# Kernel optimization log

Measured on AMD Instinct MI355X. Metric: run time of the kernel, lower is better.

Reference implementation:

```python
import jax, jax.numpy as jnp
from jax import lax
import numpy as np

B, T, F, H, L, HOR = 512, 512, 16, 256, 3, 24


def setup_inputs() -> dict:
    key = jax.random.key(0)
    ks = jax.random.split(key, 9)
    s = 0.05
    x = jax.random.normal(ks[0], (B, T, F), dtype=jnp.float32)
    # PyTorch LSTM params: gate order (i, f, g, o), W_ih [4H, in], W_hh [4H, H]
    W_ih0 = jax.random.normal(ks[1], (4 * H, F), dtype=jnp.float32) * s
    W_ih12 = jax.random.normal(ks[2], (L - 1, 4 * H, H), dtype=jnp.float32) * s
    W_hh = jax.random.normal(ks[3], (L, 4 * H, H), dtype=jnp.float32) * s
    b_ih = jax.random.normal(ks[4], (L, 4 * H), dtype=jnp.float32) * s
    b_hh = jax.random.normal(ks[5], (L, 4 * H), dtype=jnp.float32) * s
    fc_W = jax.random.normal(ks[6], (HOR, H), dtype=jnp.float32) * s
    fc_b = jax.random.normal(ks[7], (HOR,), dtype=jnp.float32) * s
    return {"x": x, "W_ih0": W_ih0, "W_ih12": W_ih12, "W_hh": W_hh,
            "b_ih": b_ih, "b_hh": b_hh, "fc_W": fc_W, "fc_b": fc_b}


def _lstm_layer(x, W_ih, W_hh, b_ih, b_hh):
    # x: [B, T, in] -> h sequence [B, T, H]
    Bn = x.shape[0]
    Hn = W_hh.shape[1]
    # precompute input contribution for all timesteps (one big GEMM)
    xg = jnp.einsum('bti,gi->btg', x, W_ih) + b_ih  # [B, T, 4H]
    W_hh_T = W_hh.T  # [H, 4H]

    def step(carry, xg_t):
        h, c = carry
        gates = xg_t + h @ W_hh_T + b_hh  # [B, 4H]
        i, f, g, o = jnp.split(gates, 4, axis=-1)
        c = jax.nn.sigmoid(f) * c + jax.nn.sigmoid(i) * jnp.tanh(g)
        h = jax.nn.sigmoid(o) * jnp.tanh(c)
        return (h, c), h

    h0 = jnp.zeros((Bn, Hn), x.dtype)
    c0 = jnp.zeros((Bn, Hn), x.dtype)
    _, hs = lax.scan(step, (h0, c0), jnp.swapaxes(xg, 0, 1))  # [T, B, H]
    return jnp.swapaxes(hs, 0, 1)


def reference(x, W_ih0, W_ih12, W_hh, b_ih, b_hh, fc_W, fc_b):
    h = _lstm_layer(x, W_ih0, W_hh[0], b_ih[0], b_hh[0])
    for l in range(1, L):
        h = _lstm_layer(h, W_ih12[l - 1], W_hh[l], b_ih[l], b_hh[l])
    last_hidden = h[:, -1, :]  # [B, H]
    return last_hidden @ fc_W.T + fc_b  # [B, horizon]
```

## Files before the change

### kernel.cpp

```cpp
#include <hip/hip_runtime.h>
#include <hip/hip_bf16.h>
#include <stdint.h>

#define Bsz 512
#define Tsz 512
#define Fsz 16
#define Hsz 256
#define HORZ 24

#define NG 8
#define NBT 8
#define BT 64
#define USL 32
#define PD 8
#define HBUF_ELEMS ((size_t)3*PD*Bsz*Hsz)
#define NFLAGS (3*NG*NBT)
#define AROW_B 512
#define ABUF_B (BT*AROW_B)
#define HTILE_B (BT*64)
#define SMEM_B (3*ABUF_B + HTILE_B)

#define POISON   0x7FC07FC0u
#define POISON64 0x7FC07FC07FC07FC0ull

typedef float  f32x4  __attribute__((ext_vector_type(4)));
typedef float  f32x16 __attribute__((ext_vector_type(16)));
typedef __bf16 bf16x8 __attribute__((ext_vector_type(8)));
typedef uint32_t u32x2 __attribute__((ext_vector_type(2)));
typedef uint32_t u32x4 __attribute__((ext_vector_type(4)));

__device__ __forceinline__ float sigm(float v){ return 1.f/(1.f+__expf(-v)); }

__device__ __forceinline__ bf16x8 ld_sc01_b128(const void* p){
  bf16x8 r;
  asm volatile("global_load_dwordx4 %0, %1, off sc0 sc1" : "=&v"(r) : "v"(p) : "memory");
  return r;
}
__device__ __forceinline__ u32x2 ld_b64_async(const void* p){
  u32x2 r;
  asm volatile("global_load_dwordx2 %0, %1, off" : "=&v"(r) : "v"(p) : "memory");
  return r;
}
__device__ __forceinline__ void st_sc01_b64(void* p, uint64_t v){
  asm volatile("global_store_dwordx2 %0, %1, off sc0 sc1" :: "v"(p), "v"(v) : "memory");
}
__device__ __forceinline__ void st_sc01_b32(void* p, uint32_t v){
  asm volatile("global_store_dword %0, %1, off sc0 sc1" :: "v"(p), "v"(v) : "memory");
}
__device__ __forceinline__ uint32_t ld_sc01_b32(const void* p){
  uint32_t r;
  asm volatile("global_load_dword %0, %1, off sc0 sc1\n\ts_waitcnt vmcnt(0)"
    : "=&v"(r) : "v"(p) : "memory");
  return r;
}
__device__ __forceinline__ void wait_flag(const unsigned int* fp, int target){
  int guard = 0;
  while ((int)ld_sc01_b32(fp) < target){
    __builtin_amdgcn_s_sleep(1);
    if (++guard > (1<<18)) break;
  }
}
__device__ __forceinline__ bool poison_free(const bf16x8* v){
  bool ok = true;
  #pragma unroll
  for (int j=0;j<4;++j){
    u32x4 uv = __builtin_bit_cast(u32x4, v[j]);
    ok = ok && (uv[0] != POISON) && (uv[2] != POISON);
  }
  return ok;
}
__device__ __forceinline__ void poll_load4(bf16x8* dst, const __bf16* src){
  int guard = 0;
  for(;;){
    #pragma unroll
    for (int j=0;j<4;++j) dst[j] = ld_sc01_b128(src + j*8);
    asm volatile("s_waitcnt vmcnt(0)" ::: "memory");
    __builtin_amdgcn_sched_barrier(0);
    if (poison_free(dst)) break;
    __builtin_amdgcn_s_sleep(1);
    if (++guard > (1<<16)) break;
  }
}

template<bool L0>
__device__ __forceinline__ void lstm_body(
    int l, int g, int nb, int tid,
    const float* __restrict__ xin,
    const float* __restrict__ Wih0,
    const float* __restrict__ Wih12,
    const float* __restrict__ Whh,
    const float* __restrict__ bih,
    const float* __restrict__ bhh,
    __bf16* __restrict__ hb,
    unsigned int* __restrict__ flags,
    char* smem)
{
  char* ain0  = smem;
  char* ain1  = smem + ABUF_B;
  char* hrc   = smem + 2*ABUF_B;
  char* htile = smem + 3*ABUF_B;

  const int lane = tid & 63;
  const int wid  = tid >> 6;
  const int wm   = wid >> 2;
  const int wn   = wid & 3;
  const int b0   = nb * BT;
  const int m0   = wm * 32;
  const int n0   = wn * 32;

  const int colL = n0 + (lane & 31);
  const int hi   = lane >> 5;
  const int kg8  = hi * 8;
  const int kg16 = hi * 16;
  const int R    = (colL&3)*Hsz + g*USL + (colL>>2);
  const float bias = bih[l*4*Hsz + R] + bhh[l*4*Hsz + R];
  const int rowA = m0 + (lane & 31);
  const int swzA = (rowA & 7) << 4;

  constexpr int NC = L0 ? 17 : 32;
  bf16x8 w[NC];
  {
    const float* recB = Whh + ((size_t)l*4*Hsz + R)*Hsz;
    #pragma unroll
    for (int c=0;c<NC;++c){
      const float* p;
      if constexpr (L0) p = (c==0) ? (Wih0 + (size_t)R*Fsz + kg8)
                                   : (recB + (c-1)*16 + kg8);
      else              p = (c<16) ? (Wih12 + ((size_t)(l-1)*4*Hsz + R)*Hsz + c*16 + kg8)
                                   : (recB + (c-16)*16 + kg8);
      f32x4 u0 = *(const f32x4*)p;
      f32x4 u1 = *(const f32x4*)(p+4);
      bf16x8 t;
      #pragma unroll
      for (int j=0;j<4;++j){ t[j]=(__bf16)u0[j]; t[j+4]=(__bf16)u1[j]; }
      w[c] = t;
    }
  }

  const int srow = tid >> 3, sq = tid & 7;
  const int sswz = (srow & 7) << 4;
  const size_t sgrow = (size_t)(b0 + srow) * Hsz;

  float cst[16];
  #pragma unroll
  for (int i=0;i<16;++i) cst[i]=0.f;

  unsigned int* myflag = flags + ((l*NG+g)*NBT + nb);
  const bool q2 = ((colL & 3) == 2);
  auto slotp = [&](int ll, int s){ return hb + ((size_t)ll*PD + (s&(PD-1)))*Bsz*Hsz; };

  {
    u32x4 z = {0,0,0,0};
    #pragma unroll
    for (int j=0;j<4;++j) *(u32x4*)(hrc + tid*64 + j*16) = z;
  }
  if constexpr (L0){
    u32x2 xv = ld_b64_async(xin + ((size_t)(b0+srow)*Tsz + 0)*Fsz + sq*2);
    asm volatile("s_waitcnt vmcnt(0)" ::: "memory");
    __builtin_amdgcn_sched_barrier(0);
    char* d = ain0 + srow*32 + sq*4;
    *(__bf16*)(d)   = (__bf16)__uint_as_float(xv[0]);
    *(__bf16*)(d+2) = (__bf16)__uint_as_float(xv[1]);
  } else {
    bf16x8 av[4];
    poll_load4(av, slotp(l-1,0) + sgrow + sq*32);
    #pragma unroll
    for (int j=0;j<4;++j)
      *(bf16x8*)(ain0 + srow*AROW_B + ((sq*64 + j*16) ^ sswz)) = av[j];
  }
  __syncthreads();

  for (int t=0; t<Tsz; ++t){
    char* aprd = (t&1) ? ain1 : ain0;
    char* apwr = (t&1) ? ain0 : ain1;

    if (l < 2 && (t & 3) == 0 && t >= 4 && tid < 8)
      wait_flag(flags + (((l+1)*NG + tid)*NBT + nb), t-3);

    bf16x8 hiv[4]; const __bf16* pfsrc = nullptr;
    const bool pfon = (!L0) && (t+1 < Tsz);
    if constexpr (L0){
      u32x2 xv = ld_b64_async(xin + ((size_t)(b0+srow)*Tsz + t)*Fsz + sq*2);
      bf16x8 hrv[4];
      if (t > 0) poll_load4(hrv, slotp(l,t-1) + sgrow + sq*32);
      else { asm volatile("s_waitcnt vmcnt(0)" ::: "memory");
             __builtin_amdgcn_sched_barrier(0); }
      char* d = ain0 + srow*32 + sq*4;
      *(__bf16*)(d)   = (__bf16)__uint_as_float(xv[0]);
      *(__bf16*)(d+2) = (__bf16)__uint_as_float(xv[1]);
      if (t > 0){
        #pragma unroll
        for (int j=0;j<4;++j)
          *(bf16x8*)(hrc + srow*AROW_B + ((sq*64 + j*16) ^ sswz)) = hrv[j];
      }
    } else {
      if (t > 0){
        bf16x8 hrv[4];
        poll_load4(hrv, slotp(l,t-1) + sgrow + sq*32);
        #pragma unroll
        for (int j=0;j<4;++j)
          *(bf16x8*)(hrc + srow*AROW_B + ((sq*64 + j*16) ^ sswz)) = hrv[j];
      }
      if (pfon){
        pfsrc = slotp(l-1,t+1) + sgrow + sq*32;
        #pragma unroll
        for (int j=0;j<4;++j) hiv[j] = ld_sc01_b128(pfsrc + j*8);
      }
    }
    __syncthreads();

    f32x16 acc;
    #pragma unroll
    for (int i=0;i<16;++i) acc[i]=0.f;
    #pragma unroll
    for (int c=0;c<NC;++c){
      bf16x8 af;
      if constexpr (L0){
        if (c==0) af = *(const bf16x8*)(ain0 + rowA*32 + kg16);
        else      af = *(const bf16x8*)(hrc + rowA*AROW_B + ((((c-1)*32) + kg16) ^ swzA));
      } else {
        if (c<16) af = *(const bf16x8*)(aprd + rowA*AROW_B + (((c*32) + kg16) ^ swzA));
        else      af = *(const bf16x8*)(hrc  + rowA*AROW_B + ((((c-16)*32) + kg16) ^ swzA));
      }
      acc = __builtin_amdgcn_mfma_f32_32x32x16_bf16(af, w[c], acc, 0,0,0);
    }

    #pragma unroll
    for (int i=0;i<16;++i){
      float v  = acc[i] + bias;
      float vv = q2 ? 2.f*v : v;
      float sg = sigm(vv);
      float act = q2 ? (2.f*sg - 1.f) : sg;
      float a1 = __shfl_xor(act,1,64);
      float a2 = __shfl_xor(act,2,64);
      float a3 = __shfl_xor(act,3,64);
      if ((lane&3)==0){
        float cn = a1*cst[i] + act*a2;
        cst[i] = cn;
        float th = 2.f*sigm(2.f*cn) - 1.f;
        float hv = a3*th;
        int r = (i&3) + 8*(i>>2) + 4*hi;
        int unit = colL >> 2;
        *(__bf16*)(htile + (m0 + r)*64 + unit*2) = (__bf16)hv;
      }
    }
    __syncthreads();

    if (pfon){
      asm volatile("s_waitcnt vmcnt(0)" ::: "memory");
      __builtin_amdgcn_sched_barrier(0);
      if (!poison_free(hiv)) poll_load4(hiv, pfsrc);
      #pragma unroll
      for (int j=0;j<4;++j)
        *(bf16x8*)(apwr + srow*AROW_B + ((sq*64 + j*16) ^ sswz)) = hiv[j];
    }
    __syncthreads();
    {
      uint64_t v = *(const uint64_t*)(htile + srow*64 + sq*8);
      st_sc01_b64(slotp(l,t)   + sgrow + g*USL + sq*4, v);
      st_sc01_b64(slotp(l,t+2) + sgrow + g*USL + sq*4, POISON64);
    }
    if (tid==0) st_sc01_b32(myflag, (uint32_t)(t+1));
  }
}

__global__ __launch_bounds__(512, 2) void lstm_persist(
    const float* __restrict__ xin,
    const float* __restrict__ Wih0,
    const float* __restrict__ Wih12,
    const float* __restrict__ Whh,
    const float* __restrict__ bih,
    const float* __restrict__ bhh,
    __bf16* __restrict__ hb,
    unsigned int* __restrict__ flags)
{
  __shared__ __align__(16) char smem[SMEM_B];
  const int bid = blockIdx.x;
  const int l   = bid >> 6;
  const int g   = (bid >> 3) & 7;
  const int nb  = bid & 7;
  const int tid = threadIdx.x;
  if (l == 0)
    lstm_body<true >(l,g,nb,tid, xin,Wih0,Wih12,Whh,bih,bhh, hb,flags, smem);
  else
    lstm_body<false>(l,g,nb,tid, xin,Wih0,Wih12,Whh,bih,bhh, hb,flags, smem);
}

__global__ void init_ws(uint32_t* __restrict__ hb32, uint32_t* __restrict__ flags)
{
  size_t i = (size_t)blockIdx.x*blockDim.x + threadIdx.x;
  size_t n = (HBUF_ELEMS*2)/16;
  if (i < n){
    u32x4 v = {POISON, POISON, POISON, POISON};
    *(u32x4*)(hb32 + i*4) = v;
  }
  if (i < NFLAGS) flags[i] = 0;
}

__global__ void fc_kernel(const __bf16* __restrict__ hb,
                          const float* __restrict__ fcW,
                          const float* __restrict__ fcb,
                          float* __restrict__ out)
{
  __shared__ float hs[Hsz];
  int b = blockIdx.x;
  const __bf16* hp = hb + ((size_t)(2*PD + ((Tsz-1)&(PD-1))))*Bsz*Hsz + (size_t)b*Hsz;
  for (int i = threadIdx.x; i < Hsz; i += 64) hs[i] = (float)hp[i];
  __syncthreads();
  int o = threadIdx.x;
  if (o < HORZ) {
    float a = fcb[o];
    #pragma unroll 8
    for (int u=0; u<Hsz; ++u) a += hs[u]*fcW[o*Hsz + u];
    out[b*HORZ + o] = a;
  }
}

extern "C" void kernel_launch(void* const* d_in, const int* in_sizes, int n_in,
                              void* d_out, int out_size, void* d_ws, size_t ws_size,
                              hipStream_t stream)
{
  const float* x     = (const float*)d_in[0];
  const float* Wih0  = (const float*)d_in[1];
  const float* Wih12 = (const float*)d_in[2];
  const float* Whh   = (const float*)d_in[3];
  const float* bih   = (const float*)d_in[4];
  const float* bhh   = (const float*)d_in[5];
  const float* fcW   = (const float*)d_in[6];
  const float* fcb   = (const float*)d_in[7];

  __bf16* hb = (__bf16*)d_ws;
  unsigned int* flags = (unsigned int*)((char*)d_ws + HBUF_ELEMS*2);

  size_t nchunk = (HBUF_ELEMS*2)/16;
  int ib = (int)((nchunk + 255) / 256);
  hipLaunchKernelGGL(init_ws, dim3(ib), dim3(256), 0, stream, (uint32_t*)hb, flags);

  hipLaunchKernelGGL(lstm_persist, dim3(3*NG*NBT), dim3(512), 0, stream,
                     x, Wih0, Wih12, Whh, bih, bhh, hb, flags);
  hipLaunchKernelGGL(fc_kernel, dim3(Bsz), dim3(64), 0, stream, hb, fcW, fcb, (float*)d_out);
}
```

Baseline: 3.283 ms.

## Halve unit groups per layer so each block computes 64 hidden units

Reduces the number of unit groups per layer from 8 to 4, so each persistent block owns 64 hidden units and all 64 batch rows. Each wave now runs two MFMA accumulators over the rows. The cell state moves from registers to shared memory. The hidden-state writeback is widened to 128-bit stores and moved before the prefetch wait. The grid shrinks to 96 blocks with fewer cross-block flags to poll, at the cost of more MFMA work per block per timestep and extra LDS traffic for the cell state.

```diff
diff --git a/kernel.cpp b/kernel.cpp
--- a/kernel.cpp
+++ b/kernel.cpp
@@ -8,17 +8,18 @@
 #define Hsz 256
 #define HORZ 24
 
-#define NG 8
+#define NG 4
 #define NBT 8
 #define BT 64
-#define USL 32
+#define USL 64
 #define PD 8
 #define HBUF_ELEMS ((size_t)3*PD*Bsz*Hsz)
 #define NFLAGS (3*NG*NBT)
 #define AROW_B 512
 #define ABUF_B (BT*AROW_B)
-#define HTILE_B (BT*64)
-#define SMEM_B (3*ABUF_B + HTILE_B)
+#define HTILE_B (BT*128)
+#define CST_B (BT*USL*4)
+#define SMEM_B (3*ABUF_B + HTILE_B + CST_B)
 
 #define POISON   0x7FC07FC0u
 #define POISON64 0x7FC07FC07FC07FC0ull
@@ -41,8 +42,8 @@
   asm volatile("global_load_dwordx2 %0, %1, off" : "=&v"(r) : "v"(p) : "memory");
   return r;
 }
-__device__ __forceinline__ void st_sc01_b64(void* p, uint64_t v){
-  asm volatile("global_store_dwordx2 %0, %1, off sc0 sc1" :: "v"(p), "v"(v) : "memory");
+__device__ __forceinline__ void st_sc01_b128(void* p, u32x4 v){
+  asm volatile("global_store_dwordx4 %0, %1, off sc0 sc1" :: "v"(p), "v"(v) : "memory");
 }
 __device__ __forceinline__ void st_sc01_b32(void* p, uint32_t v){
   asm volatile("global_store_dword %0, %1, off sc0 sc1" :: "v"(p), "v"(v) : "memory");
@@ -99,23 +100,23 @@
   char* ain1  = smem + ABUF_B;
   char* hrc   = smem + 2*ABUF_B;
   char* htile = smem + 3*ABUF_B;
+  float* cstp = (float*)(smem + 3*ABUF_B + HTILE_B);
 
   const int lane = tid & 63;
   const int wid  = tid >> 6;
-  const int wm   = wid >> 2;
-  const int wn   = wid & 3;
   const int b0   = nb * BT;
-  const int m0   = wm * 32;
-  const int n0   = wn * 32;
-
-  const int colL = n0 + (lane & 31);
+
+  const int colL = wid*32 + (lane & 31);
   const int hi   = lane >> 5;
   const int kg8  = hi * 8;
   const int kg16 = hi * 16;
-  const int R    = (colL&3)*Hsz + g*USL + (colL>>2);
+  const int gate = colL & 3;
+  const int unitL = colL >> 2;
+  const int R    = gate*Hsz + g*USL + unitL;
   const float bias = bih[l*4*Hsz + R] + bhh[l*4*Hsz + R];
-  const int rowA = m0 + (lane & 31);
+  const int rowA = lane & 31;
   const int swzA = (rowA & 7) << 4;
+  const bool q2 = (gate == 2);
 
   constexpr int NC = L0 ? 17 : 32;
   bf16x8 w[NC];
@@ -141,18 +142,15 @@
   const int sswz = (srow & 7) << 4;
   const size_t sgrow = (size_t)(b0 + srow) * Hsz;
 
-  float cst[16];
-  #pragma unroll
-  for (int i=0;i<16;++i) cst[i]=0.f;
-
   unsigned int* myflag = flags + ((l*NG+g)*NBT + nb);
-  const bool q2 = ((colL & 3) == 2);
   auto slotp = [&](int ll, int s){ return hb + ((size_t)ll*PD + (s&(PD-1)))*Bsz*Hsz; };
 
   {
     u32x4 z = {0,0,0,0};
     #pragma unroll
     for (int j=0;j<4;++j) *(u32x4*)(hrc + tid*64 + j*16) = z;
+    *(u32x4*)((char*)cstp + tid*32)      = z;
+    *(u32x4*)((char*)cstp + tid*32 + 16) = z;
   }
   if constexpr (L0){
     u32x2 xv = ld_b64_async(xin + ((size_t)(b0+srow)*Tsz + 0)*Fsz + sq*2);
@@ -171,14 +169,14 @@
   __syncthreads();
 
   for (int t=0; t<Tsz; ++t){
+    if (l < 2 && (t & 3) == 0 && t >= 4 && tid < NG)
+      wait_flag(flags + (((l+1)*NG + tid)*NBT + nb), t-3);
+
     char* aprd = (t&1) ? ain1 : ain0;
     char* apwr = (t&1) ? ain0 : ain1;
-
-    if (l < 2 && (t & 3) == 0 && t >= 4 && tid < 8)
-      wait_flag(flags + (((l+1)*NG + tid)*NBT + nb), t-3);
-
     bf16x8 hiv[4]; const __bf16* pfsrc = nullptr;
     const bool pfon = (!L0) && (t+1 < Tsz);
+
     if constexpr (L0){
       u32x2 xv = ld_b64_async(xin + ((size_t)(b0+srow)*Tsz + t)*Fsz + sq*2);
       bf16x8 hrv[4];
@@ -209,57 +207,69 @@
     }
     __syncthreads();
 
-    f32x16 acc;
-    #pragma unroll
-    for (int i=0;i<16;++i) acc[i]=0.f;
+    f32x16 acc0, acc1;
+    #pragma unroll
+    for (int i=0;i<16;++i){ acc0[i]=0.f; acc1[i]=0.f; }
     #pragma unroll
     for (int c=0;c<NC;++c){
-      bf16x8 af;
+      bf16x8 a0, a1;
       if constexpr (L0){
-        if (c==0) af = *(const bf16x8*)(ain0 + rowA*32 + kg16);
-        else      af = *(const bf16x8*)(hrc + rowA*AROW_B + ((((c-1)*32) + kg16) ^ swzA));
+        if (c==0){ a0 = *(const bf16x8*)(ain0 + rowA*32 + kg16);
+                   a1 = *(const bf16x8*)(ain0 + (rowA+32)*32 + kg16); }
+        else { int off = (((c-1)*32) + kg16) ^ swzA;
+               a0 = *(const bf16x8*)(hrc + rowA*AROW_B + off);
+               a1 = *(const bf16x8*)(hrc + (rowA+32)*AROW_B + off); }
       } else {
-        if (c<16) af = *(const bf16x8*)(aprd + rowA*AROW_B + (((c*32) + kg16) ^ swzA));
-        else      af = *(const bf16x8*)(hrc  + rowA*AROW_B + ((((c-16)*32) + kg16) ^ swzA));
-      }
-      acc = __builtin_amdgcn_mfma_f32_32x32x16_bf16(af, w[c], acc, 0,0,0);
-    }
-
-    #pragma unroll
-    for (int i=0;i<16;++i){
-      float v  = acc[i] + bias;
-      float vv = q2 ? 2.f*v : v;
-      float sg = sigm(vv);
-      float act = q2 ? (2.f*sg - 1.f) : sg;
-      float a1 = __shfl_xor(act,1,64);
-      float a2 = __shfl_xor(act,2,64);
-      float a3 = __shfl_xor(act,3,64);
-      if ((lane&3)==0){
-        float cn = a1*cst[i] + act*a2;
-        cst[i] = cn;
-        float th = 2.f*sigm(2.f*cn) - 1.f;
-        float hv = a3*th;
-        int r = (i&3) + 8*(i>>2) + 4*hi;
-        int unit = colL >> 2;
-        *(__bf16*)(htile + (m0 + r)*64 + unit*2) = (__bf16)hv;
+        const char* bse = (c<16) ? aprd : hrc;
+        int cc = (c<16) ? c : c-16;
+        int off = ((cc*32) + kg16) ^ swzA;
+        a0 = *(const bf16x8*)(bse + rowA*AROW_B + off);
+        a1 = *(const bf16x8*)(bse + (rowA+32)*AROW_B + off);
+      }
+      acc0 = __builtin_amdgcn_mfma_f32_32x32x16_bf16(a0, w[c], acc0, 0,0,0);
+      acc1 = __builtin_amdgcn_mfma_f32_32x32x16_bf16(a1, w[c], acc1, 0,0,0);
+    }
+
+    #pragma unroll
+    for (int mt=0; mt<2; ++mt){
+      #pragma unroll
+      for (int i=0;i<16;++i){
+        float v  = (mt ? acc1[i] : acc0[i]) + bias;
+        float vv = q2 ? 2.f*v : v;
+        float sg = sigm(vv);
+        float act = q2 ? (2.f*sg - 1.f) : sg;
+        float a1 = __shfl_xor(act,1,64);
+        float a2 = __shfl_xor(act,2,64);
+        float a3 = __shfl_xor(act,3,64);
+        if (gate==0){
+          int r = (i&3) + 8*(i>>2) + 4*hi;
+          int idx = (mt*32 + r)*64 + unitL;
+          float cn = a1*cstp[idx] + act*a2;
+          cstp[idx] = cn;
+          float th = 2.f*sigm(2.f*cn) - 1.f;
+          float hv = a3*th;
+          *(__bf16*)(htile + (mt*32 + r)*128 + unitL*2) = (__bf16)hv;
+        }
       }
     }
     __syncthreads();
 
+    {
+      int row = tid>>3, q = tid&7;
+      u32x4 v = *(const u32x4*)(htile + row*128 + q*16);
+      u32x4 pz = {POISON,POISON,POISON,POISON};
+      st_sc01_b128(slotp(l,t)   + (size_t)(b0+row)*Hsz + g*USL + q*8, v);
+      st_sc01_b128(slotp(l,t+2) + (size_t)(b0+row)*Hsz + g*USL + q*8, pz);
+    }
+    asm volatile("s_waitcnt vmcnt(0)" ::: "memory");
+    __builtin_amdgcn_sched_barrier(0);
     if (pfon){
-      asm volatile("s_waitcnt vmcnt(0)" ::: "memory");
-      __builtin_amdgcn_sched_barrier(0);
       if (!poison_free(hiv)) poll_load4(hiv, pfsrc);
       #pragma unroll
       for (int j=0;j<4;++j)
         *(bf16x8*)(apwr + srow*AROW_B + ((sq*64 + j*16) ^ sswz)) = hiv[j];
     }
     __syncthreads();
-    {
-      uint64_t v = *(const uint64_t*)(htile + srow*64 + sq*8);
-      st_sc01_b64(slotp(l,t)   + sgrow + g*USL + sq*4, v);
-      st_sc01_b64(slotp(l,t+2) + sgrow + g*USL + sq*4, POISON64);
-    }
     if (tid==0) st_sc01_b32(myflag, (uint32_t)(t+1));
   }
 }
@@ -276,8 +286,8 @@
 {
   __shared__ __align__(16) char smem[SMEM_B];
   const int bid = blockIdx.x;
-  const int l   = bid >> 6;
-  const int g   = (bid >> 3) & 7;
+  const int l   = bid >> 5;
+  const int g   = (bid >> 3) & 3;
   const int nb  = bid & 7;
   const int tid = threadIdx.x;
   if (l == 0)
```

New measurement: 6.795 ms. +107.0%, slower.
